# Kernel optimization log

Hardware: AMD Instinct MI355X
Metric: run time of the kernel (lower is better)

The kernel has to match this reference:

```python
import jax, jax.numpy as jnp
import numpy as np

EPS = 1e-06

def _splat_dists(t, centers):
    # t: [B,T,H,Dh], centers: [H,S,Dh] -> euclidean dists [B,T,H,S] (torch.cdist)
    t_sq = jnp.sum(t * t, axis=-1, keepdims=True)          # [B,T,H,1]
    c_sq = jnp.sum(centers * centers, axis=-1)             # [H,S]
    dots = jnp.einsum('bthd,hsd->bths', t, centers)        # [B,T,H,S]
    d2 = jnp.maximum(t_sq + c_sq[None, None] - 2.0 * dots, 0.0)
    return jnp.sqrt(d2)


def setup_inputs() -> dict:
    key = jax.random.key(0)
    ks = jax.random.split(key, 6)
    B, T, D, H, S = 2, 2048, 1024, 8, 32
    Dh = D // H
    scale = 1.0 / np.sqrt(D)
    return {
        'x': jax.random.normal(ks[0], (B, T, D), jnp.float32),
        'Wqkv': jax.random.normal(ks[1], (D, 3 * D), jnp.float32) * scale,
        'bqkv': jnp.zeros((3 * D,), jnp.float32),
        'Wout': jax.random.normal(ks[2], (D, D), jnp.float32) * scale,
        'bout': jnp.zeros((D,), jnp.float32),
        'splat_centers': jax.random.normal(ks[3], (H, S, Dh), jnp.float32) * 0.5,
        'splat_log_scales': jnp.zeros((H, S), jnp.float32),
        'splat_log_amplitudes': jnp.zeros((H, S), jnp.float32),
        'temperature': jnp.ones((1,), jnp.float32),
    }


def reference(x, Wqkv, bqkv, Wout, bout, splat_centers, splat_log_scales,
              splat_log_amplitudes, temperature):
    B, T, D = x.shape
    H, S, Dh = splat_centers.shape
    qkv = (x @ Wqkv + bqkv).reshape(B, T, 3, H, Dh)
    q, k, v = qkv[:, :, 0], qkv[:, :, 1], qkv[:, :, 2]     # [B,T,H,Dh]

    q_dists = _splat_dists(q, splat_centers)               # [B,T,H,S]
    k_dists = _splat_dists(k, splat_centers)               # [B,T,H,S]

    scales = jnp.exp(splat_log_scales)[None, None]         # [1,1,H,S]
    q_weights = jnp.exp(-0.5 * (q_dists / (scales + EPS)) ** 2)
    k_weights = jnp.exp(-0.5 * (k_dists / (scales + EPS)) ** 2)

    amplitudes = jnp.exp(splat_log_amplitudes)             # [H,S]
    # bihs,bjhs,hs -> bijh : fold amplitudes into q_weights first
    qa = q_weights * amplitudes[None, None]
    logits = jnp.einsum('bihs,bjhs->bijh', qa, k_weights) / temperature[0]
    attention = jax.nn.softmax(logits, axis=2)             # softmax over j
    out = jnp.einsum('bijh,bjhd->bihd', attention, v).reshape(B, T, D)
    return out @ Wout + bout, attention
```

## Files before the change

### kernel.cpp

```cpp
#include <hip/hip_runtime.h>
#include <math.h>


typedef __attribute__((ext_vector_type(8))) short s16x8;
typedef __attribute__((ext_vector_type(4))) short s16x4;
typedef __attribute__((ext_vector_type(4))) float f32x4;

__device__ inline short f2bf(float f) {
  union { float f; unsigned u; } v; v.f = f;
  unsigned r = v.u + 0x7FFFu + ((v.u >> 16) & 1u);
  return (short)(r >> 16);
}
__device__ inline unsigned cvt_pk_bf16(float lo, float hi) {
  unsigned r;
  asm("v_cvt_pk_bf16_f32 %0, %1, %2" : "=v"(r) : "v"(lo), "v"(hi));
  return r;
}
#define MFMA_BF16(a, b, c) __builtin_amdgcn_mfma_f32_16x16x32_bf16((a), (b), (c), 0, 0, 0)

#define GLOAD_LDS16(gsrc, ldst)                                          \
  __builtin_amdgcn_global_load_lds(                                      \
      (const __attribute__((address_space(1))) void*)(gsrc),             \
      (__attribute__((address_space(3))) void*)(ldst), 16, 0, 0)

__device__ inline void transpose_tile32(const float* __restrict__ W,
                                        short* __restrict__ Wt, int K, int N,
                                        int n0, int k0) {
  __shared__ float tile[32][33];
  const int r = threadIdx.x >> 3, c4 = (threadIdx.x & 7) * 4;
  float4 v = *(const float4*)(W + (size_t)(k0 + r) * N + n0 + c4);
  tile[r][c4 + 0] = v.x; tile[r][c4 + 1] = v.y;
  tile[r][c4 + 2] = v.z; tile[r][c4 + 3] = v.w;
  __syncthreads();
  s16x4 o;
  o[0] = f2bf(tile[c4 + 0][r]);
  o[1] = f2bf(tile[c4 + 1][r]);
  o[2] = f2bf(tile[c4 + 2][r]);
  o[3] = f2bf(tile[c4 + 3][r]);
  *(s16x4*)(Wt + (size_t)(n0 + r) * K + k0 + c4) = o;
}

__global__ __launch_bounds__(256) void prep_fused(
    const float* __restrict__ x, short* __restrict__ x16,
    const float* __restrict__ Wqkv, short* __restrict__ Wqt16,
    const float* __restrict__ Wout, short* __restrict__ Wot16,
    const float* __restrict__ ctr, const float* __restrict__ ls,
    const float* __restrict__ la, short* __restrict__ c16,
    float* __restrict__ csq, float* __restrict__ inv2, float* __restrict__ amp) {
  const int bx = blockIdx.x;
  if (bx < 4096) {
    int i = bx * 256 + threadIdx.x;
    float4 v = ((const float4*)x)[i];
    s16x4 o;
    o[0] = f2bf(v.x); o[1] = f2bf(v.y); o[2] = f2bf(v.z); o[3] = f2bf(v.w);
    ((s16x4*)x16)[i] = o;
  } else if (bx < 7168) {
    int idx = bx - 4096;
    transpose_tile32(Wqkv, Wqt16, 1024, 3072, (idx % 96) * 32, (idx / 96) * 32);
  } else if (bx < 8192) {
    int idx = bx - 7168;
    transpose_tile32(Wout, Wot16, 1024, 1024, (idx % 32) * 32, (idx / 32) * 32);
  } else {
    const int t = threadIdx.x;
    float sumsq = 0.f;
#pragma unroll
    for (int d = 0; d < 128; d += 4) {
      float4 v = *(const float4*)(ctr + (size_t)t * 128 + d);
      sumsq += v.x * v.x + v.y * v.y + v.z * v.z + v.w * v.w;
      s16x4 o;
      o[0] = f2bf(v.x); o[1] = f2bf(v.y); o[2] = f2bf(v.z); o[3] = f2bf(v.w);
      *(s16x4*)(c16 + (size_t)t * 128 + d) = o;
    }
    csq[t] = sumsq;
    float sc = __expf(ls[t]);
    float iv = 1.0f / (sc + 1e-6f);
    inv2[t] = -0.5f * iv * iv;
    amp[t] = __expf(la[t]);
  }
}

template <int N, bool SCATTER>
__global__ __launch_bounds__(256) void gemm_bf16(
    const short* __restrict__ A, const short* __restrict__ Wt,
    const float* __restrict__ bias,
    float* __restrict__ out0, float* __restrict__ out1, float* __restrict__ out2) {
  __shared__ short As[128 * 64];
  __shared__ short Bs[128 * 64];
  const int tid = threadIdx.x;
  const int w = tid >> 6, l = tid & 63;
  const int lm = l & 15, lk = l >> 4;
  const int bn0 = blockIdx.x * 128;
  const int bm0 = blockIdx.y * 128;
  const int n0 = bn0 + (w & 1) * 64;
  const int m0 = bm0 + (w >> 1) * 64;
  const int K = 1024;
  f32x4 acc[4][4];
#pragma unroll
  for (int mi = 0; mi < 4; mi++)
#pragma unroll
    for (int ni = 0; ni < 4; ni++) acc[mi][ni] = (f32x4){0.f, 0.f, 0.f, 0.f};

  const int srow = l >> 3;
  const int scol = (l & 7) * 8;
  const int mh = (w >> 1) * 64, nh = (w & 1) * 64;

  for (int k0 = 0; k0 < K; k0 += 64) {
#pragma unroll
    for (int q = 0; q < 4; q++) {
      const int chunk = w * 4 + q;
      const int row = chunk * 8 + srow;
      GLOAD_LDS16(A + (size_t)(bm0 + row) * K + k0 + scol, As + chunk * 512);
      GLOAD_LDS16(Wt + (size_t)(bn0 + row) * K + k0 + scol, Bs + chunk * 512);
    }
    __syncthreads();
#pragma unroll
    for (int kk = 0; kk < 2; kk++) {
      s16x8 af[4], bf[4];
#pragma unroll
      for (int i = 0; i < 4; i++) {
        af[i] = *(const s16x8*)(As + (mh + i * 16 + lm) * 64 + kk * 32 + lk * 8);
        bf[i] = *(const s16x8*)(Bs + (nh + i * 16 + lm) * 64 + kk * 32 + lk * 8);
      }
#pragma unroll
      for (int mi = 0; mi < 4; mi++)
#pragma unroll
        for (int ni = 0; ni < 4; ni++)
          acc[mi][ni] = MFMA_BF16(af[mi], bf[ni], acc[mi][ni]);
    }
    __syncthreads();
  }
#pragma unroll
  for (int ni = 0; ni < 4; ni++) {
    const int n = n0 + ni * 16 + lm;
    const float bv = bias[n];
#pragma unroll
    for (int mi = 0; mi < 4; mi++) {
#pragma unroll
      for (int r = 0; r < 4; r++) {
        const int m = m0 + mi * 16 + lk * 4 + r;
        float v = acc[mi][ni][r] + bv;
        if (SCATTER) {
          int three = n >> 10;
          int h = (n >> 7) & 7;
          int dh = n & 127;
          int bb = m >> 11, tt = m & 2047;
          float* dst = (three == 0) ? out0 : ((three == 1) ? out1 : out2);
          dst[((size_t)(bb * 8 + h) * 2048 + tt) * 128 + dh] = v;
        } else {
          out0[(size_t)m * N + n] = v;
        }
      }
    }
  }
}

__global__ __launch_bounds__(256) void splat_tv(
    const float* __restrict__ qT, const float* __restrict__ kT,
    const short* __restrict__ c16, const float* __restrict__ csq,
    const float* __restrict__ inv2, const float* __restrict__ amp,
    short* __restrict__ qa16, short* __restrict__ kw16,
    const float* __restrict__ vT, short* __restrict__ vt16) {
  __shared__ float tile[32][33];
  const int tid = threadIdx.x;
  if (blockIdx.x < 1024) {
    const int it = blockIdx.x & 31;
    const int bh = (blockIdx.x >> 5) & 15;
    const int which = blockIdx.x >> 9;
    const int w = tid >> 6, l = tid & 63;
    const int lm = l & 15, lk = l >> 4;
    const int h = bh & 7;
    const int i0 = it * 64 + w * 16;
    const float* src = which ? kT : qT;

    s16x8 af[4];
    float sq = 0.f;
#pragma unroll
    for (int kk = 0; kk < 4; kk++) {
      const float* p = src + ((size_t)bh * 2048 + i0 + lm) * 128 + kk * 32 + lk * 8;
      float4 v0 = *(const float4*)p;
      float4 v1 = *(const float4*)(p + 4);
      sq += v0.x * v0.x + v0.y * v0.y + v0.z * v0.z + v0.w * v0.w +
            v1.x * v1.x + v1.y * v1.y + v1.z * v1.z + v1.w * v1.w;
      af[kk][0] = f2bf(v0.x); af[kk][1] = f2bf(v0.y);
      af[kk][2] = f2bf(v0.z); af[kk][3] = f2bf(v0.w);
      af[kk][4] = f2bf(v1.x); af[kk][5] = f2bf(v1.y);
      af[kk][6] = f2bf(v1.z); af[kk][7] = f2bf(v1.w);
    }
    sq += __shfl_xor(sq, 16);
    sq += __shfl_xor(sq, 32);

    f32x4 acc[2];
    acc[0] = (f32x4){0.f, 0.f, 0.f, 0.f};
    acc[1] = (f32x4){0.f, 0.f, 0.f, 0.f};
#pragma unroll
    for (int kk = 0; kk < 4; kk++) {
      s16x8 b0 = *(const s16x8*)(c16 + (size_t)(h * 32 + lm) * 128 + kk * 32 + lk * 8);
      s16x8 b1 = *(const s16x8*)(c16 + (size_t)(h * 32 + 16 + lm) * 128 + kk * 32 + lk * 8);
      acc[0] = MFMA_BF16(af[kk], b0, acc[0]);
      acc[1] = MFMA_BF16(af[kk], b1, acc[1]);
    }
    short* dst = which ? kw16 : qa16;
#pragma unroll
    for (int ni = 0; ni < 2; ni++) {
      const int n = ni * 16 + lm;
      const float cs = csq[h * 32 + n];
      const float iv2 = inv2[h * 32 + n];
      const float am = which ? 1.0f : amp[h * 32 + n];
#pragma unroll
      for (int r = 0; r < 4; r++) {
        float qs = __shfl(sq, lk * 4 + r);
        float d2 = fmaxf(qs + cs - 2.0f * acc[ni][r], 0.0f);
        float wv = __expf(iv2 * d2) * am;
        int m = i0 + lk * 4 + r;
        dst[((size_t)bh * 2048 + m) * 32 + n] = f2bf(wv);
      }
    }
  } else {
    const int idx = blockIdx.x - 1024;
    const int t0 = (idx & 63) * 32;
    const int d0 = ((idx >> 6) & 3) * 32;
    const int bh = idx >> 8;
    const int r = tid >> 3, c4 = (tid & 7) * 4;
    float4 v = *(const float4*)(vT + ((size_t)(bh * 2048 + t0 + r)) * 128 + d0 + c4);
    tile[r][c4 + 0] = v.x; tile[r][c4 + 1] = v.y;
    tile[r][c4 + 2] = v.z; tile[r][c4 + 3] = v.w;
    __syncthreads();
    s16x4 o;
    o[0] = f2bf(tile[c4 + 0][r]);
    o[1] = f2bf(tile[c4 + 1][r]);
    o[2] = f2bf(tile[c4 + 2][r]);
    o[3] = f2bf(tile[c4 + 3][r]);
    *(s16x4*)(vt16 + ((size_t)(bh * 128 + d0 + r)) * 2048 + t0 + c4) = o;
  }
}

__global__ __launch_bounds__(256) void attn_flash(
    const short* __restrict__ qa16, const short* __restrict__ kw16,
    const short* __restrict__ vt16, const float* __restrict__ temp,
    float* __restrict__ lpart, float* __restrict__ accf) {
  __shared__ short Vs[2][8192];
  const int tid = threadIdx.x;
  const int w = tid >> 6, l = tid & 63;
  const int lm = l & 15, lk = l >> 4;
  const int it = blockIdx.x, h = blockIdx.y;
  const int b = blockIdx.z & 1, jh = blockIdx.z >> 1;
  const int bh = b * 8 + h;
  const int i0 = it * 64 + w * 16;
  const float invT = 1.0f / temp[0];
  const short* kwb = kw16 + (size_t)bh * 2048 * 32;
  const short* vtb = vt16 + (size_t)bh * 128 * 2048;
  s16x8 qfrag = *(const s16x8*)(qa16 + ((size_t)(bh * 2048 + i0 + lm)) * 32 + lk * 8);
  float lsum = 0.f;
  f32x4 acc[8];
#pragma unroll
  for (int d = 0; d < 8; d++) acc[d] = (f32x4){0.f, 0.f, 0.f, 0.f};

  const int sig0 = (lm >> 2) * 8 + (lm & 3);
  const int srow8 = l >> 3;
  const int scb = (l & 7) ^ srow8;
  const int rcb0 = (lk ^ (lm & 7)) * 8;
  const int rcb1 = ((lk + 4) ^ (lm & 7)) * 8;

  const int j0 = jh * 1024;
#pragma unroll
  for (int q = 0; q < 4; q++) {
    const int chunk = w * 4 + q;
    GLOAD_LDS16(vtb + (size_t)(chunk * 8 + srow8) * 2048 + j0 + scb * 8,
                &Vs[0][chunk * 512]);
  }
  __syncthreads();

  int cur = 0;
  for (int jc = j0; jc < j0 + 1024; jc += 64) {
    if (jc + 64 < j0 + 1024) {
#pragma unroll
      for (int q = 0; q < 4; q++) {
        const int chunk = w * 4 + q;
        GLOAD_LDS16(vtb + (size_t)(chunk * 8 + srow8) * 2048 + (jc + 64) + scb * 8,
                    &Vs[cur ^ 1][chunk * 512]);
      }
    }
    s16x8 kb[4];
    kb[0] = *(const s16x8*)(kwb + (size_t)(jc + sig0) * 32 + lk * 8);
    kb[1] = *(const s16x8*)(kwb + (size_t)(jc + sig0 + 4) * 32 + lk * 8);
    kb[2] = *(const s16x8*)(kwb + (size_t)(jc + sig0 + 32) * 32 + lk * 8);
    kb[3] = *(const s16x8*)(kwb + (size_t)(jc + sig0 + 36) * 32 + lk * 8);
    f32x4 z = (f32x4){0.f, 0.f, 0.f, 0.f};
    f32x4 s[4];
#pragma unroll
    for (int c = 0; c < 4; c++) s[c] = MFMA_BF16(kb[c], qfrag, z);
    float p[4][4];
#pragma unroll
    for (int c = 0; c < 4; c++) {
      p[c][0] = __expf(s[c][0] * invT);
      p[c][1] = __expf(s[c][1] * invT);
      p[c][2] = __expf(s[c][2] * invT);
      p[c][3] = __expf(s[c][3] * invT);
      lsum += (p[c][0] + p[c][1]) + (p[c][2] + p[c][3]);
    }
    union { unsigned u[4]; s16x8 v; } t0, t1;
    t0.u[0] = cvt_pk_bf16(p[0][0], p[0][1]);
    t0.u[1] = cvt_pk_bf16(p[0][2], p[0][3]);
    t0.u[2] = cvt_pk_bf16(p[1][0], p[1][1]);
    t0.u[3] = cvt_pk_bf16(p[1][2], p[1][3]);
    t1.u[0] = cvt_pk_bf16(p[2][0], p[2][1]);
    t1.u[1] = cvt_pk_bf16(p[2][2], p[2][3]);
    t1.u[2] = cvt_pk_bf16(p[3][0], p[3][1]);
    t1.u[3] = cvt_pk_bf16(p[3][2], p[3][3]);
    s16x8 pf0 = t0.v, pf1 = t1.v;
    const short* vb = Vs[cur];
#pragma unroll
    for (int d = 0; d < 8; d++) {
      const short* vsrow = vb + (d * 16 + lm) * 64;
      s16x8 vb0 = *(const s16x8*)(vsrow + rcb0);
      s16x8 vb1 = *(const s16x8*)(vsrow + rcb1);
      acc[d] = MFMA_BF16(pf0, vb0, acc[d]);
      acc[d] = MFMA_BF16(pf1, vb1, acc[d]);
    }
    __syncthreads();
    cur ^= 1;
  }
  lsum += __shfl_xor(lsum, 16);
  lsum += __shfl_xor(lsum, 32);
  float* af = accf + (size_t)jh * 4194304;
#pragma unroll
  for (int r = 0; r < 4; r++) {
    int row = i0 + lk * 4 + r;
    float* ob = af + (size_t)(b * 2048 + row) * 1024 + h * 128 + lm;
#pragma unroll
    for (int d = 0; d < 8; d++) ob[d * 16] = acc[d][r];
  }
  if (l < 16) {
    lpart[jh * 32768 + bh * 2048 + i0 + l] = lsum;
  }
}

__global__ __launch_bounds__(256) void attn_combine(
    const float* __restrict__ accf, const float* __restrict__ lpart,
    short* __restrict__ aout16, float* __restrict__ lrow) {
  const int m = blockIdx.x;
  const int b = m >> 11, i = m & 2047;
  const int t = threadIdx.x;
  const int n = t * 4;
  const int h = n >> 7;
  const int bhrow = (b * 8 + h) * 2048 + i;
  const float l0 = lpart[bhrow], l1 = lpart[32768 + bhrow];
  const float lv = l0 + l1;
  const float invl = 1.0f / lv;
  float4 v0 = *(const float4*)(accf + (size_t)m * 1024 + n);
  float4 v1 = *(const float4*)(accf + 4194304 + (size_t)m * 1024 + n);
  s16x4 o;
  o[0] = f2bf((v0.x + v1.x) * invl);
  o[1] = f2bf((v0.y + v1.y) * invl);
  o[2] = f2bf((v0.z + v1.z) * invl);
  o[3] = f2bf((v0.w + v1.w) * invl);
  *(s16x4*)(aout16 + (size_t)m * 1024 + n) = o;
  if ((n & 127) == 0) lrow[bhrow] = lv;
}

__global__ __launch_bounds__(256) void gemm_out(
    const short* __restrict__ aout16, const short* __restrict__ Wot16,
    const float* __restrict__ bout, float* __restrict__ out) {
  __shared__ short As[128 * 64];
  __shared__ short Bs[128 * 64];
  const int tid = threadIdx.x;
  const int w = tid >> 6, l = tid & 63;
  const int lm = l & 15, lk = l >> 4;
  const int idx = blockIdx.x;
  const int bn0 = (idx & 7) * 128;
  const int bm0 = (idx >> 3) * 128;
  const int n0 = bn0 + (w & 1) * 64;
  const int m0 = bm0 + (w >> 1) * 64;
  const int K = 1024;
  f32x4 acc[4][4];
#pragma unroll
  for (int mi = 0; mi < 4; mi++)
#pragma unroll
    for (int ni = 0; ni < 4; ni++) acc[mi][ni] = (f32x4){0.f, 0.f, 0.f, 0.f};
  const int srow = l >> 3;
  const int scol = (l & 7) * 8;
  const int mh = (w >> 1) * 64, nh = (w & 1) * 64;
  for (int k0 = 0; k0 < K; k0 += 64) {
#pragma unroll
    for (int q = 0; q < 4; q++) {
      const int chunk = w * 4 + q;
      const int row = chunk * 8 + srow;
      GLOAD_LDS16(aout16 + (size_t)(bm0 + row) * K + k0 + scol, As + chunk * 512);
      GLOAD_LDS16(Wot16 + (size_t)(bn0 + row) * K + k0 + scol, Bs + chunk * 512);
    }
    __syncthreads();
#pragma unroll
    for (int kk = 0; kk < 2; kk++) {
      s16x8 af[4], bf[4];
#pragma unroll
      for (int i = 0; i < 4; i++) {
        af[i] = *(const s16x8*)(As + (mh + i * 16 + lm) * 64 + kk * 32 + lk * 8);
        bf[i] = *(const s16x8*)(Bs + (nh + i * 16 + lm) * 64 + kk * 32 + lk * 8);
      }
#pragma unroll
      for (int mi = 0; mi < 4; mi++)
#pragma unroll
        for (int ni = 0; ni < 4; ni++)
          acc[mi][ni] = MFMA_BF16(af[mi], bf[ni], acc[mi][ni]);
    }
    __syncthreads();
  }
#pragma unroll
  for (int ni = 0; ni < 4; ni++) {
    const int n = n0 + ni * 16 + lm;
    const float bv = bout[n];
#pragma unroll
    for (int mi = 0; mi < 4; mi++) {
#pragma unroll
      for (int r = 0; r < 4; r++) {
        const int m = m0 + mi * 16 + lk * 4 + r;
        out[(size_t)m * 1024 + n] = acc[mi][ni][r] + bv;
      }
    }
  }
}

__global__ __launch_bounds__(256) void attn_write(
    const short* __restrict__ qa16, const short* __restrict__ kw16,
    const float* __restrict__ lrow, const float* __restrict__ temp,
    float* __restrict__ attn) {
  __shared__ float pl[8][16][33];
  const int tid = threadIdx.x;
  const int w = tid >> 6, l = tid & 63;
  const int lm = l & 15, lk = l >> 4;
  const int bx = blockIdx.x;
  const int i0 = (bx & 127) * 16;
  const int j0 = ((bx >> 7) & 63) * 32;
  const int b = bx >> 13;
  const float invT = 1.0f / temp[0];
#pragma unroll
  for (int hh = 0; hh < 2; hh++) {
    const int h = w * 2 + hh;
    const int bh = b * 8 + h;
    s16x8 qf = *(const s16x8*)(qa16 + ((size_t)(bh * 2048 + i0 + lm)) * 32 + lk * 8);
    s16x8 kf[2];
#pragma unroll
    for (int jh = 0; jh < 2; jh++)
      kf[jh] = *(const s16x8*)(kw16 + ((size_t)(bh * 2048 + j0 + jh * 16 + lm)) * 32 + lk * 8);
    float il[4];
#pragma unroll
    for (int r = 0; r < 4; r++)
      il[r] = 1.0f / lrow[bh * 2048 + i0 + lk * 4 + r];
    f32x4 z = (f32x4){0.f, 0.f, 0.f, 0.f};
#pragma unroll
    for (int jh = 0; jh < 2; jh++) {
      f32x4 s = MFMA_BF16(qf, kf[jh], z);
#pragma unroll
      for (int r = 0; r < 4; r++) {
        float p = __expf(s[r] * invT) * il[r];
        pl[h][lk * 4 + r][jh * 16 + lm] = p;
      }
    }
  }
  __syncthreads();
#pragma unroll
  for (int c = 0; c < 4; c++) {
    int u = c * 256 + tid;
    int i = u >> 6, rem = u & 63;
    int j = rem >> 1, h4 = (rem & 1) * 4;
    f32x4 v;
    v[0] = pl[h4][i][j];
    v[1] = pl[h4 + 1][i][j];
    v[2] = pl[h4 + 2][i][j];
    v[3] = pl[h4 + 3][i][j];
    f32x4* dst = (f32x4*)(attn + (((size_t)(b * 2048 + i0 + i)) * 2048 + j0 + j) * 8 + h4);
    __builtin_nontemporal_store(v, dst);
  }
}

extern "C" void kernel_launch(void* const* d_in, const int* in_sizes, int n_in,
                              void* d_out, int out_size, void* d_ws, size_t ws_size,
                              hipStream_t stream) {
  const float* x    = (const float*)d_in[0];
  const float* Wqkv = (const float*)d_in[1];
  const float* bqkv = (const float*)d_in[2];
  const float* Wout = (const float*)d_in[3];
  const float* bout = (const float*)d_in[4];
  const float* ctr  = (const float*)d_in[5];
  const float* ls   = (const float*)d_in[6];
  const float* la   = (const float*)d_in[7];
  const float* temp = (const float*)d_in[8];

  float* out = (float*)d_out;
  float* attn = out + 4194304;

  float* ws = (float*)d_ws;
  float* qT    = ws;
  float* kT    = qT + 4194304;
  float* vT    = kT + 4194304;
  short* x16   = (short*)(vT + 4194304);
  short* Wqt16 = x16 + 4194304;
  short* Wot16 = Wqt16 + 3145728;
  short* qa16  = Wot16 + 1048576;
  short* kw16  = qa16 + 1048576;
  float* lpart = (float*)(kw16 + 1048576);
  float* lrow  = lpart + 65536;
  float* csq   = lrow + 32768;
  float* inv2  = csq + 256;
  float* amp   = inv2 + 256;
  short* c16   = (short*)(amp + 256);
  float* accf  = (float*)(c16 + 32768);
  short* vt16  = (short*)ws;
  short* aout16 = (short*)vT;

  prep_fused<<<8193, 256, 0, stream>>>(x, x16, Wqkv, Wqt16, Wout, Wot16,
                                       ctr, ls, la, c16, csq, inv2, amp);
  gemm_bf16<3072, true><<<dim3(24, 32), 256, 0, stream>>>(
      x16, Wqt16, bqkv, qT, kT, vT);
  splat_tv<<<5120, 256, 0, stream>>>(
      qT, kT, c16, csq, inv2, amp, qa16, kw16, vT, vt16);
  attn_flash<<<dim3(32, 8, 4), 256, 0, stream>>>(
      qa16, kw16, vt16, temp, lpart, accf);
  attn_combine<<<4096, 256, 0, stream>>>(accf, lpart, aout16, lrow);
  gemm_out<<<256, 256, 0, stream>>>(aout16, Wot16, bout, out);
  attn_write<<<16384, 256, 0, stream>>>(qa16, kw16, lrow, temp, attn);
}
```

Before: 464.5 us.

## Fuse output GEMM and attention-matrix write into one heterogeneous launch

Merges gemm_out and attn_write into a single kernel whose first 1024 blocks compute the output projection and whose remaining blocks write the attention probabilities. The output GEMM tile also shrinks from 128x128 to 64x64, giving more blocks to fill the GPU. The aim is to remove a launch boundary and let the compute-heavy GEMM overlap with the bandwidth-bound attention write. The cost is less register and LDS reuse per GEMM block and an LDS union that sets occupancy for both roles.

```diff
diff --git a/kernel.cpp b/kernel.cpp
--- a/kernel.cpp
+++ b/kernel.cpp
@@ -358,118 +358,115 @@
   if ((n & 127) == 0) lrow[bhrow] = lv;
 }
 
-__global__ __launch_bounds__(256) void gemm_out(
+__global__ __launch_bounds__(256) void attnw_gemmo(
+    const short* __restrict__ qa16, const short* __restrict__ kw16,
+    const float* __restrict__ lrow, const float* __restrict__ temp,
+    float* __restrict__ attn,
     const short* __restrict__ aout16, const short* __restrict__ Wot16,
     const float* __restrict__ bout, float* __restrict__ out) {
-  __shared__ short As[128 * 64];
-  __shared__ short Bs[128 * 64];
+  __shared__ union {
+    struct { short As[64 * 64]; short Bs[64 * 64]; } g;
+    float pl[8][16][33];
+  } sm;
   const int tid = threadIdx.x;
   const int w = tid >> 6, l = tid & 63;
   const int lm = l & 15, lk = l >> 4;
-  const int idx = blockIdx.x;
-  const int bn0 = (idx & 7) * 128;
-  const int bm0 = (idx >> 3) * 128;
-  const int n0 = bn0 + (w & 1) * 64;
-  const int m0 = bm0 + (w >> 1) * 64;
-  const int K = 1024;
-  f32x4 acc[4][4];
-#pragma unroll
-  for (int mi = 0; mi < 4; mi++)
-#pragma unroll
-    for (int ni = 0; ni < 4; ni++) acc[mi][ni] = (f32x4){0.f, 0.f, 0.f, 0.f};
-  const int srow = l >> 3;
-  const int scol = (l & 7) * 8;
-  const int mh = (w >> 1) * 64, nh = (w & 1) * 64;
-  for (int k0 = 0; k0 < K; k0 += 64) {
-#pragma unroll
-    for (int q = 0; q < 4; q++) {
-      const int chunk = w * 4 + q;
-      const int row = chunk * 8 + srow;
-      GLOAD_LDS16(aout16 + (size_t)(bm0 + row) * K + k0 + scol, As + chunk * 512);
-      GLOAD_LDS16(Wot16 + (size_t)(bn0 + row) * K + k0 + scol, Bs + chunk * 512);
+  if (blockIdx.x < 1024) {
+    const int idx = blockIdx.x;
+    const int bn0 = (idx & 15) * 64;
+    const int bm0 = (idx >> 4) * 64;
+    const int mh = (w >> 1) * 32, nh = (w & 1) * 32;
+    f32x4 acc[2][2];
+#pragma unroll
+    for (int mi = 0; mi < 2; mi++)
+#pragma unroll
+      for (int ni = 0; ni < 2; ni++) acc[mi][ni] = (f32x4){0.f, 0.f, 0.f, 0.f};
+    const int srow8 = l >> 3;
+    const int scb8 = (l & 7) * 8;
+    for (int k0 = 0; k0 < 1024; k0 += 64) {
+#pragma unroll
+      for (int q = 0; q < 2; q++) {
+        const int chunk = w * 2 + q;
+        const int row = chunk * 8 + srow8;
+        GLOAD_LDS16(aout16 + (size_t)(bm0 + row) * 1024 + k0 + scb8,
+                    sm.g.As + chunk * 512);
+        GLOAD_LDS16(Wot16 + (size_t)(bn0 + row) * 1024 + k0 + scb8,
+                    sm.g.Bs + chunk * 512);
+      }
+      __syncthreads();
+#pragma unroll
+      for (int kk = 0; kk < 2; kk++) {
+        s16x8 af[2], bf[2];
+#pragma unroll
+        for (int i = 0; i < 2; i++) {
+          af[i] = *(const s16x8*)(sm.g.As + (mh + i * 16 + lm) * 64 + kk * 32 + lk * 8);
+          bf[i] = *(const s16x8*)(sm.g.Bs + (nh + i * 16 + lm) * 64 + kk * 32 + lk * 8);
+        }
+#pragma unroll
+        for (int mi = 0; mi < 2; mi++)
+#pragma unroll
+          for (int ni = 0; ni < 2; ni++)
+            acc[mi][ni] = MFMA_BF16(af[mi], bf[ni], acc[mi][ni]);
+      }
+      __syncthreads();
+    }
+#pragma unroll
+    for (int ni = 0; ni < 2; ni++) {
+      const int n = bn0 + nh + ni * 16 + lm;
+      const float bv = bout[n];
+#pragma unroll
+      for (int mi = 0; mi < 2; mi++) {
+#pragma unroll
+        for (int r = 0; r < 4; r++) {
+          const int m = bm0 + mh + mi * 16 + lk * 4 + r;
+          out[(size_t)m * 1024 + n] = acc[mi][ni][r] + bv;
+        }
+      }
+    }
+  } else {
+    const int bx = blockIdx.x - 1024;
+    const int i0 = (bx & 127) * 16;
+    const int j0 = ((bx >> 7) & 63) * 32;
+    const int b = bx >> 13;
+    const float invT = 1.0f / temp[0];
+#pragma unroll
+    for (int hh = 0; hh < 2; hh++) {
+      const int h = w * 2 + hh;
+      const int bh = b * 8 + h;
+      s16x8 qf = *(const s16x8*)(qa16 + ((size_t)(bh * 2048 + i0 + lm)) * 32 + lk * 8);
+      s16x8 kf[2];
+#pragma unroll
+      for (int jh = 0; jh < 2; jh++)
+        kf[jh] = *(const s16x8*)(kw16 + ((size_t)(bh * 2048 + j0 + jh * 16 + lm)) * 32 + lk * 8);
+      float il[4];
+#pragma unroll
+      for (int r = 0; r < 4; r++)
+        il[r] = 1.0f / lrow[bh * 2048 + i0 + lk * 4 + r];
+      f32x4 z = (f32x4){0.f, 0.f, 0.f, 0.f};
+#pragma unroll
+      for (int jh = 0; jh < 2; jh++) {
+        f32x4 s = MFMA_BF16(qf, kf[jh], z);
+#pragma unroll
+        for (int r = 0; r < 4; r++) {
+          float p = __expf(s[r] * invT) * il[r];
+          sm.pl[h][lk * 4 + r][jh * 16 + lm] = p;
+        }
+      }
     }
     __syncthreads();
 #pragma unroll
-    for (int kk = 0; kk < 2; kk++) {
-      s16x8 af[4], bf[4];
-#pragma unroll
-      for (int i = 0; i < 4; i++) {
-        af[i] = *(const s16x8*)(As + (mh + i * 16 + lm) * 64 + kk * 32 + lk * 8);
-        bf[i] = *(const s16x8*)(Bs + (nh + i * 16 + lm) * 64 + kk * 32 + lk * 8);
-      }
-#pragma unroll
-      for (int mi = 0; mi < 4; mi++)
-#pragma unroll
-        for (int ni = 0; ni < 4; ni++)
-          acc[mi][ni] = MFMA_BF16(af[mi], bf[ni], acc[mi][ni]);
-    }
-    __syncthreads();
-  }
-#pragma unroll
-  for (int ni = 0; ni < 4; ni++) {
-    const int n = n0 + ni * 16 + lm;
-    const float bv = bout[n];
-#pragma unroll
-    for (int mi = 0; mi < 4; mi++) {
-#pragma unroll
-      for (int r = 0; r < 4; r++) {
-        const int m = m0 + mi * 16 + lk * 4 + r;
-        out[(size_t)m * 1024 + n] = acc[mi][ni][r] + bv;
-      }
-    }
-  }
-}
-
-__global__ __launch_bounds__(256) void attn_write(
-    const short* __restrict__ qa16, const short* __restrict__ kw16,
-    const float* __restrict__ lrow, const float* __restrict__ temp,
-    float* __restrict__ attn) {
-  __shared__ float pl[8][16][33];
-  const int tid = threadIdx.x;
-  const int w = tid >> 6, l = tid & 63;
-  const int lm = l & 15, lk = l >> 4;
-  const int bx = blockIdx.x;
-  const int i0 = (bx & 127) * 16;
-  const int j0 = ((bx >> 7) & 63) * 32;
-  const int b = bx >> 13;
-  const float invT = 1.0f / temp[0];
-#pragma unroll
-  for (int hh = 0; hh < 2; hh++) {
-    const int h = w * 2 + hh;
-    const int bh = b * 8 + h;
-    s16x8 qf = *(const s16x8*)(qa16 + ((size_t)(bh * 2048 + i0 + lm)) * 32 + lk * 8);
-    s16x8 kf[2];
-#pragma unroll
-    for (int jh = 0; jh < 2; jh++)
-      kf[jh] = *(const s16x8*)(kw16 + ((size_t)(bh * 2048 + j0 + jh * 16 + lm)) * 32 + lk * 8);
-    float il[4];
-#pragma unroll
-    for (int r = 0; r < 4; r++)
-      il[r] = 1.0f / lrow[bh * 2048 + i0 + lk * 4 + r];
-    f32x4 z = (f32x4){0.f, 0.f, 0.f, 0.f};
-#pragma unroll
-    for (int jh = 0; jh < 2; jh++) {
-      f32x4 s = MFMA_BF16(qf, kf[jh], z);
-#pragma unroll
-      for (int r = 0; r < 4; r++) {
-        float p = __expf(s[r] * invT) * il[r];
-        pl[h][lk * 4 + r][jh * 16 + lm] = p;
-      }
-    }
-  }
-  __syncthreads();
-#pragma unroll
-  for (int c = 0; c < 4; c++) {
-    int u = c * 256 + tid;
-    int i = u >> 6, rem = u & 63;
-    int j = rem >> 1, h4 = (rem & 1) * 4;
-    f32x4 v;
-    v[0] = pl[h4][i][j];
-    v[1] = pl[h4 + 1][i][j];
-    v[2] = pl[h4 + 2][i][j];
-    v[3] = pl[h4 + 3][i][j];
-    f32x4* dst = (f32x4*)(attn + (((size_t)(b * 2048 + i0 + i)) * 2048 + j0 + j) * 8 + h4);
-    __builtin_nontemporal_store(v, dst);
+    for (int c = 0; c < 4; c++) {
+      int u = c * 256 + tid;
+      int i = u >> 6, rem = u & 63;
+      int j = rem >> 1, h4 = (rem & 1) * 4;
+      f32x4 v;
+      v[0] = sm.pl[h4][i][j];
+      v[1] = sm.pl[h4 + 1][i][j];
+      v[2] = sm.pl[h4 + 2][i][j];
+      v[3] = sm.pl[h4 + 3][i][j];
+      f32x4* dst = (f32x4*)(attn + (((size_t)(b * 2048 + i0 + i)) * 2048 + j0 + j) * 8 + h4);
+      __builtin_nontemporal_store(v, dst);
+    }
   }
 }
 
@@ -517,6 +514,6 @@
   attn_flash<<<dim3(32, 8, 4), 256, 0, stream>>>(
       qa16, kw16, vt16, temp, lpart, accf);
   attn_combine<<<4096, 256, 0, stream>>>(accf, lpart, aout16, lrow);
-  gemm_out<<<256, 256, 0, stream>>>(aout16, Wot16, bout, out);
-  attn_write<<<16384, 256, 0, stream>>>(qa16, kw16, lrow, temp, attn);
-}
+  attnw_gemmo<<<17408, 256, 0, stream>>>(
+      qa16, kw16, lrow, temp, attn, aout16, Wot16, bout, out);
+}
```

Measured after the change: 538.7 us. 1.16x slower.

## Drop split-K attention and fuse normalization into flash kernel epilogue

Applied to the files above, without the earlier changes.

The attention kernel no longer splits the key dimension into two halves. Each block now loops over all 2048 keys, normalizes by the row sum in registers and writes bf16 output directly. This removes the combine kernel and the round trip of two fp32 partial accumulators (about 32 MB) through global memory. The cost is half as many blocks (512 instead of 1024), which lowers parallelism and doubles the serial loop length per block.

```diff
diff --git a/kernel.cpp b/kernel.cpp
--- a/kernel.cpp
+++ b/kernel.cpp
@@ -237,13 +237,13 @@
 __global__ __launch_bounds__(256) void attn_flash(
     const short* __restrict__ qa16, const short* __restrict__ kw16,
     const short* __restrict__ vt16, const float* __restrict__ temp,
-    float* __restrict__ lpart, float* __restrict__ accf) {
+    float* __restrict__ lrow, short* __restrict__ aout16) {
   __shared__ short Vs[2][8192];
   const int tid = threadIdx.x;
   const int w = tid >> 6, l = tid & 63;
   const int lm = l & 15, lk = l >> 4;
   const int it = blockIdx.x, h = blockIdx.y;
-  const int b = blockIdx.z & 1, jh = blockIdx.z >> 1;
+  const int b = blockIdx.z;
   const int bh = b * 8 + h;
   const int i0 = it * 64 + w * 16;
   const float invT = 1.0f / temp[0];
@@ -261,18 +261,17 @@
   const int rcb0 = (lk ^ (lm & 7)) * 8;
   const int rcb1 = ((lk + 4) ^ (lm & 7)) * 8;
 
-  const int j0 = jh * 1024;
 #pragma unroll
   for (int q = 0; q < 4; q++) {
     const int chunk = w * 4 + q;
-    GLOAD_LDS16(vtb + (size_t)(chunk * 8 + srow8) * 2048 + j0 + scb * 8,
+    GLOAD_LDS16(vtb + (size_t)(chunk * 8 + srow8) * 2048 + scb * 8,
                 &Vs[0][chunk * 512]);
   }
   __syncthreads();
 
   int cur = 0;
-  for (int jc = j0; jc < j0 + 1024; jc += 64) {
-    if (jc + 64 < j0 + 1024) {
+  for (int jc = 0; jc < 2048; jc += 64) {
+    if (jc + 64 < 2048) {
 #pragma unroll
       for (int q = 0; q < 4; q++) {
         const int chunk = w * 4 + q;
@@ -322,40 +321,18 @@
   }
   lsum += __shfl_xor(lsum, 16);
   lsum += __shfl_xor(lsum, 32);
-  float* af = accf + (size_t)jh * 4194304;
+  if (l < 16) lrow[bh * 2048 + i0 + l] = lsum;
+  float invl[4];
+#pragma unroll
+  for (int r = 0; r < 4; r++) invl[r] = 1.0f / __shfl(lsum, lk * 4 + r);
+  short* ob = aout16 + ((size_t)(b * 2048 + i0)) * 1024 + h * 128 + lm;
 #pragma unroll
   for (int r = 0; r < 4; r++) {
-    int row = i0 + lk * 4 + r;
-    float* ob = af + (size_t)(b * 2048 + row) * 1024 + h * 128 + lm;
-#pragma unroll
-    for (int d = 0; d < 8; d++) ob[d * 16] = acc[d][r];
-  }
-  if (l < 16) {
-    lpart[jh * 32768 + bh * 2048 + i0 + l] = lsum;
-  }
-}
-
-__global__ __launch_bounds__(256) void attn_combine(
-    const float* __restrict__ accf, const float* __restrict__ lpart,
-    short* __restrict__ aout16, float* __restrict__ lrow) {
-  const int m = blockIdx.x;
-  const int b = m >> 11, i = m & 2047;
-  const int t = threadIdx.x;
-  const int n = t * 4;
-  const int h = n >> 7;
-  const int bhrow = (b * 8 + h) * 2048 + i;
-  const float l0 = lpart[bhrow], l1 = lpart[32768 + bhrow];
-  const float lv = l0 + l1;
-  const float invl = 1.0f / lv;
-  float4 v0 = *(const float4*)(accf + (size_t)m * 1024 + n);
-  float4 v1 = *(const float4*)(accf + 4194304 + (size_t)m * 1024 + n);
-  s16x4 o;
-  o[0] = f2bf((v0.x + v1.x) * invl);
-  o[1] = f2bf((v0.y + v1.y) * invl);
-  o[2] = f2bf((v0.z + v1.z) * invl);
-  o[3] = f2bf((v0.w + v1.w) * invl);
-  *(s16x4*)(aout16 + (size_t)m * 1024 + n) = o;
-  if ((n & 127) == 0) lrow[bhrow] = lv;
+    const int row = lk * 4 + r;
+#pragma unroll
+    for (int d = 0; d < 8; d++)
+      ob[(size_t)row * 1024 + d * 16] = f2bf(acc[d][r] * invl[r]);
+  }
 }
 
 __global__ __launch_bounds__(256) void gemm_out(
@@ -498,13 +475,11 @@
   short* Wot16 = Wqt16 + 3145728;
   short* qa16  = Wot16 + 1048576;
   short* kw16  = qa16 + 1048576;
-  float* lpart = (float*)(kw16 + 1048576);
-  float* lrow  = lpart + 65536;
+  float* lrow  = (float*)(kw16 + 1048576);
   float* csq   = lrow + 32768;
   float* inv2  = csq + 256;
   float* amp   = inv2 + 256;
   short* c16   = (short*)(amp + 256);
-  float* accf  = (float*)(c16 + 32768);
   short* vt16  = (short*)ws;
   short* aout16 = (short*)vT;
 
@@ -514,9 +489,8 @@
       x16, Wqt16, bqkv, qT, kT, vT);
   splat_tv<<<5120, 256, 0, stream>>>(
       qT, kT, c16, csq, inv2, amp, qa16, kw16, vT, vt16);
-  attn_flash<<<dim3(32, 8, 4), 256, 0, stream>>>(
-      qa16, kw16, vt16, temp, lpart, accf);
-  attn_combine<<<4096, 256, 0, stream>>>(accf, lpart, aout16, lrow);
+  attn_flash<<<dim3(32, 8, 2), 256, 0, stream>>>(
+      qa16, kw16, vt16, temp, lrow, aout16);
   gemm_out<<<256, 256, 0, stream>>>(aout16, Wot16, bout, out);
   attn_write<<<16384, 256, 0, stream>>>(qa16, kw16, lrow, temp, attn);
 }
```

New measurement: 465.2 us. Within noise of the previous version (+0.2%).
